# Performance work log

Hardware: AMD Instinct MI355X
Metric: run time of the kernel (lower is better)

Reference implementation:

```python
import jax, jax.numpy as jnp
import numpy as np

H = 1024
S = 32768

def setup_inputs() -> dict:
    key = jax.random.key(0)
    k1, k2, k3, k4 = jax.random.split(key, 4)
    return {
        "hidden_state": jax.random.normal(k1, (1, 1, H), dtype=jnp.float32),
        "encoder_output": jax.random.normal(k2, (1, S, H), dtype=jnp.float32),
        "W": jax.random.normal(k3, (H, H), dtype=jnp.float32) / np.sqrt(H),
        "b": jax.random.normal(k4, (H,), dtype=jnp.float32) * 0.01,
    }

def reference(hidden_state, encoder_output, W, b):
    # method == 'general': energy_i = h . (W @ e_i + b)
    h = hidden_state[0, 0]            # [H]
    enc = encoder_output[0]           # [S, H]
    proj = enc @ W.T + b              # [S, H]  (nn.Linear)
    energies = proj @ h               # [S]
    return jax.nn.softmax(energies[None, :], axis=1)  # [1, S]
```

## Files before the change

kernel.cpp:

```cpp
#include <hip/hip_runtime.h>


#define H 1024
#define S 32768

__global__ __launch_bounds__(256) void matvec_v(const float* __restrict__ W,
                                                const float* __restrict__ h,
                                                float* __restrict__ v) {
    __shared__ float sh[64];
    const int t    = threadIdx.x;
    const int kk   = t & 15;
    const int jj   = t >> 4;
    const int w    = t >> 6;
    const int lane = t & 63;
    const int k0   = blockIdx.x * 16;

    const float* Wp = W + (size_t)jj * H + k0 + kk;
    float a0 = 0.f, a1 = 0.f;
#pragma unroll
    for (int i = 0; i < 64; i += 2) {
        a0 = fmaf(Wp[(size_t)(16 * i) * H],       h[16 * i + jj],       a0);
        a1 = fmaf(Wp[(size_t)(16 * (i + 1)) * H], h[16 * (i + 1) + jj], a1);
    }
    float a = a0 + a1;
    a += __shfl_xor(a, 16, 64);
    a += __shfl_xor(a, 32, 64);
    if (lane < 16) sh[w * 16 + lane] = a;
    __syncthreads();
    if (t < 16) v[k0 + t] = sh[t] + sh[t + 16] + sh[t + 32] + sh[t + 48];
}

__global__ __launch_bounds__(256) void energies_kernel(const float* __restrict__ enc,
                                                       const float* __restrict__ v,
                                                       float* __restrict__ e) {
    const int wave  = threadIdx.x >> 6;
    const int lane  = threadIdx.x & 63;
    const int lane4 = lane * 4;

    float4 vf[4];
#pragma unroll
    for (int t = 0; t < 4; ++t)
        vf[t] = *(const float4*)(v + t * 256 + lane4);

    const int row0 = (blockIdx.x * 4 + wave) * 4;
    const float* rp = enc + (size_t)row0 * H + lane4;

    float4 a[4][4];
#pragma unroll
    for (int r = 0; r < 4; ++r)
#pragma unroll
        for (int t = 0; t < 4; ++t)
            a[r][t] = *(const float4*)(rp + (size_t)r * H + t * 256);

    float acc[4];
#pragma unroll
    for (int r = 0; r < 4; ++r) {
        float s = 0.f;
#pragma unroll
        for (int t = 0; t < 4; ++t) {
            s = fmaf(a[r][t].x, vf[t].x, s);
            s = fmaf(a[r][t].y, vf[t].y, s);
            s = fmaf(a[r][t].z, vf[t].z, s);
            s = fmaf(a[r][t].w, vf[t].w, s);
        }
#pragma unroll
        for (int off = 32; off >= 1; off >>= 1)
            s += __shfl_xor(s, off, 64);
        acc[r] = s;
    }
    if (lane == 0)
        *(float4*)(e + row0) = make_float4(acc[0], acc[1], acc[2], acc[3]);
}

__global__ __launch_bounds__(1024) void softmax_kernel(const float* __restrict__ e,
                                                       float* __restrict__ out) {
    __shared__ float red[16];
    const int t    = threadIdx.x;
    const int lane = t & 63;
    const int wv   = t >> 6;

    float4 x[8];
#pragma unroll
    for (int r = 0; r < 8; ++r)
        x[r] = *(const float4*)(e + 4 * t + 4096 * r);

    float m = -1e30f;
#pragma unroll
    for (int r = 0; r < 8; ++r)
        m = fmaxf(m, fmaxf(fmaxf(x[r].x, x[r].y), fmaxf(x[r].z, x[r].w)));
#pragma unroll
    for (int off = 32; off >= 1; off >>= 1)
        m = fmaxf(m, __shfl_xor(m, off, 64));
    if (lane == 0) red[wv] = m;
    __syncthreads();
    if (t < 16) {
        float mm = red[t];
#pragma unroll
        for (int off = 8; off >= 1; off >>= 1)
            mm = fmaxf(mm, __shfl_xor(mm, off, 64));
        if (t == 0) red[0] = mm;
    }
    __syncthreads();
    m = red[0];
    __syncthreads();

    float s = 0.f;
#pragma unroll
    for (int r = 0; r < 8; ++r) {
        x[r].x = __expf(x[r].x - m); s += x[r].x;
        x[r].y = __expf(x[r].y - m); s += x[r].y;
        x[r].z = __expf(x[r].z - m); s += x[r].z;
        x[r].w = __expf(x[r].w - m); s += x[r].w;
    }
#pragma unroll
    for (int off = 32; off >= 1; off >>= 1)
        s += __shfl_xor(s, off, 64);
    if (lane == 0) red[wv] = s;
    __syncthreads();
    if (t < 16) {
        float ss = red[t];
#pragma unroll
        for (int off = 8; off >= 1; off >>= 1)
            ss += __shfl_xor(ss, off, 64);
        if (t == 0) red[0] = ss;
    }
    __syncthreads();
    const float inv = 1.0f / red[0];

#pragma unroll
    for (int r = 0; r < 8; ++r) {
        float4 y;
        y.x = x[r].x * inv;
        y.y = x[r].y * inv;
        y.z = x[r].z * inv;
        y.w = x[r].w * inv;
        *(float4*)(out + 4 * t + 4096 * r) = y;
    }
}

extern "C" void kernel_launch(void* const* d_in, const int* in_sizes, int n_in,
                              void* d_out, int out_size, void* d_ws, size_t ws_size,
                              hipStream_t stream) {
    const float* h   = (const float*)d_in[0];
    const float* enc = (const float*)d_in[1];
    const float* W   = (const float*)d_in[2];

    float* v = (float*)d_ws;
    float* e = (float*)d_ws + H;
    float* out = (float*)d_out;

    matvec_v<<<64, 256, 0, stream>>>(W, h, v);
    energies_kernel<<<S / 16, 256, 0, stream>>>(enc, v, e);
    softmax_kernel<<<1, 1024, 0, stream>>>(e, out);
}
```

Before: 207.2 us.

## Fuse matvec, energies and softmax into one cooperative kernel with grid syncs

Replaces the three launches with a single cooperative kernel of 256 blocks. Each block computes a partial W^T h slice, then after a grid sync streams 128 encoder rows and keeps their energies in shared memory. The softmax is done as a two-pass distributed max/sum across blocks with further grid syncs, which removes the launch gaps and the single-block softmax tail. The cost is three grid-wide barriers, and only 256 blocks are left to stream 128 MB of encoder data, which may lower memory-level parallelism compared with 2048 blocks.

```diff
diff --git a/kernel.cpp b/kernel.cpp
--- a/kernel.cpp
+++ b/kernel.cpp
@@ -1,8 +1,177 @@
 #include <hip/hip_runtime.h>
+#include <hip/hip_cooperative_groups.h>
+
+namespace cg = cooperative_groups;
 
 
 #define H 1024
 #define S 32768
+#define NB 256
+#define NT 512
+#define RPB (S / NB)
+
+__global__ __launch_bounds__(NT) void fused_attn(const float* __restrict__ W,
+                                                 const float* __restrict__ h,
+                                                 const float* __restrict__ enc,
+                                                 float* __restrict__ out,
+                                                 float* __restrict__ ws) {
+    cg::grid_group grid = cg::this_grid();
+    __shared__ float sh[RPB];
+    __shared__ float red[16];
+
+    const int b    = blockIdx.x;
+    const int t    = threadIdx.x;
+    const int lane = t & 63;
+    const int wave = t >> 6;
+
+    float* vpart = ws;
+    float* wmax  = ws + 4 * H;
+    float* wsum  = ws + 4 * H + NB;
+
+    {
+        const int kb = b >> 2;
+        const int jg = b & 3;
+        const int k0 = kb * 16;
+        const int kk = t & 15;
+        const int jj = t >> 4;
+        const float* Wp = W + (size_t)(jg * 256 + jj) * H + k0 + kk;
+        const float* hp = h + jg * 256 + jj;
+        float a0 = 0.f, a1 = 0.f;
+#pragma unroll
+        for (int i = 0; i < 8; i += 2) {
+            a0 = fmaf(Wp[(size_t)(32 * i) * H],       hp[32 * i],       a0);
+            a1 = fmaf(Wp[(size_t)(32 * (i + 1)) * H], hp[32 * (i + 1)], a1);
+        }
+        float a = a0 + a1;
+        a += __shfl_xor(a, 16, 64);
+        a += __shfl_xor(a, 32, 64);
+        if (lane < 16) sh[wave * 16 + lane] = a;
+        __syncthreads();
+        if (t < 16) {
+            float s = 0.f;
+#pragma unroll
+            for (int wv = 0; wv < 8; ++wv) s += sh[wv * 16 + t];
+            vpart[jg * H + k0 + t] = s;
+        }
+    }
+    grid.sync();
+
+    const int lane4 = lane * 4;
+    float4 vf[4];
+#pragma unroll
+    for (int tt = 0; tt < 4; ++tt) {
+        float4 s0 = *(const float4*)(vpart + 0 * H + tt * 256 + lane4);
+        float4 s1 = *(const float4*)(vpart + 1 * H + tt * 256 + lane4);
+        float4 s2 = *(const float4*)(vpart + 2 * H + tt * 256 + lane4);
+        float4 s3 = *(const float4*)(vpart + 3 * H + tt * 256 + lane4);
+        vf[tt].x = (s0.x + s1.x) + (s2.x + s3.x);
+        vf[tt].y = (s0.y + s1.y) + (s2.y + s3.y);
+        vf[tt].z = (s0.z + s1.z) + (s2.z + s3.z);
+        vf[tt].w = (s0.w + s1.w) + (s2.w + s3.w);
+    }
+
+#pragma unroll
+    for (int it = 0; it < 4; ++it) {
+        const int lrow = wave * 16 + it * 4;
+        const float* rp = enc + (size_t)(b * RPB + lrow) * H + lane4;
+        float4 a[4][4];
+#pragma unroll
+        for (int r = 0; r < 4; ++r)
+#pragma unroll
+            for (int tt = 0; tt < 4; ++tt)
+                a[r][tt] = *(const float4*)(rp + (size_t)r * H + tt * 256);
+#pragma unroll
+        for (int r = 0; r < 4; ++r) {
+            float s = 0.f;
+#pragma unroll
+            for (int tt = 0; tt < 4; ++tt) {
+                s = fmaf(a[r][tt].x, vf[tt].x, s);
+                s = fmaf(a[r][tt].y, vf[tt].y, s);
+                s = fmaf(a[r][tt].z, vf[tt].z, s);
+                s = fmaf(a[r][tt].w, vf[tt].w, s);
+            }
+#pragma unroll
+            for (int off = 32; off >= 1; off >>= 1)
+                s += __shfl_xor(s, off, 64);
+            if (lane == 0) sh[lrow + r] = s;
+        }
+    }
+    __syncthreads();
+
+    {
+        float lm = (t < RPB) ? sh[t] : -3.0e38f;
+#pragma unroll
+        for (int off = 32; off >= 1; off >>= 1)
+            lm = fmaxf(lm, __shfl_xor(lm, off, 64));
+        if (lane == 0) red[wave] = lm;
+        __syncthreads();
+        if (t == 0) {
+            float m = red[0];
+#pragma unroll
+            for (int wv = 1; wv < 8; ++wv) m = fmaxf(m, red[wv]);
+            wmax[b] = m;
+        }
+    }
+    grid.sync();
+
+    float gm;
+    {
+        float m = (t < NB) ? wmax[t] : -3.0e38f;
+#pragma unroll
+        for (int off = 32; off >= 1; off >>= 1)
+            m = fmaxf(m, __shfl_xor(m, off, 64));
+        if (lane == 0) red[wave] = m;
+        __syncthreads();
+        if (t == 0) {
+            float mm = red[0];
+#pragma unroll
+            for (int wv = 1; wv < 8; ++wv) mm = fmaxf(mm, red[wv]);
+            red[8] = mm;
+        }
+        __syncthreads();
+        gm = red[8];
+    }
+
+    {
+        float p = 0.f;
+        if (t < RPB) {
+            p = __expf(sh[t] - gm);
+            sh[t] = p;
+        }
+        float s = p;
+#pragma unroll
+        for (int off = 32; off >= 1; off >>= 1)
+            s += __shfl_xor(s, off, 64);
+        if (lane == 0) red[wave] = s;
+        __syncthreads();
+        if (t == 0) {
+            float Z = red[0];
+#pragma unroll
+            for (int wv = 1; wv < 8; ++wv) Z += red[wv];
+            wsum[b] = Z;
+        }
+    }
+    grid.sync();
+
+    {
+        float z = (t < NB) ? wsum[t] : 0.f;
+#pragma unroll
+        for (int off = 32; off >= 1; off >>= 1)
+            z += __shfl_xor(z, off, 64);
+        if (lane == 0) red[wave] = z;
+        __syncthreads();
+        if (t == 0) {
+            float Z = red[0];
+#pragma unroll
+            for (int wv = 1; wv < 8; ++wv) Z += red[wv];
+            red[8] = 1.0f / Z;
+        }
+        __syncthreads();
+        const float inv = red[8];
+        if (t < RPB) out[b * RPB + t] = sh[t] * inv;
+    }
+}
+
 
 __global__ __launch_bounds__(256) void matvec_v(const float* __restrict__ W,
                                                 const float* __restrict__ h,
@@ -145,11 +314,17 @@
     const float* enc = (const float*)d_in[1];
     const float* W   = (const float*)d_in[2];
 
-    float* v = (float*)d_ws;
-    float* e = (float*)d_ws + H;
     float* out = (float*)d_out;
-
-    matvec_v<<<64, 256, 0, stream>>>(W, h, v);
-    energies_kernel<<<S / 16, 256, 0, stream>>>(enc, v, e);
-    softmax_kernel<<<1, 1024, 0, stream>>>(e, out);
-}
+    float* ws  = (float*)d_ws;
+
+    void* args[] = {(void*)&W, (void*)&h, (void*)&enc, (void*)&out, (void*)&ws};
+    hipError_t err = hipLaunchCooperativeKernel((void*)fused_attn, dim3(NB), dim3(NT),
+                                                args, 0, stream);
+    if (err != hipSuccess) {
+        float* v = ws;
+        float* e = ws + H;
+        matvec_v<<<64, 256, 0, stream>>>(W, h, v);
+        energies_kernel<<<S / 16, 256, 0, stream>>>(enc, v, e);
+        softmax_kernel<<<1, 1024, 0, stream>>>(e, out);
+    }
+}
```

Result: slower. 287.4 us (+38.7%).
